# Kernel tuning notes

Hardware: AMD Instinct MI355X
Metric: run time of the kernel (lower is better)

The kernel has to match this reference:

```python
import jax, jax.numpy as jnp
import numpy as np

P = 32      # process_dim (event types)
H = 1024    # hidden_size
T = 128     # sequence length
B = 128     # batch size


def setup_inputs() -> dict:
    key = jax.random.key(0)
    k_dt, k_ty, k_e, k_w, k_b = jax.random.split(key, 5)
    seq_dt = jax.random.uniform(k_dt, (T, B), dtype=jnp.float32)
    seq_types = jax.random.randint(k_ty, (T, B), 0, P, dtype=jnp.int32)
    h0 = jnp.zeros((B, H), jnp.float32)
    c0 = jnp.zeros((B, H), jnp.float32)
    # Embedding: P+1 rows, padding row (index P) zeroed as in nn.Embedding(padding_idx=P)
    embed = (jax.random.normal(k_e, (P + 1, P), jnp.float32) * 0.02).at[P].set(0.0)
    # 7 gate Linears fused into one weight: order = [input, forget, output,
    # input_target, forget_target, z, decay]; torch Linear is y = v @ W^T + b,
    # here W is stored pre-transposed as [P+H, 7H].
    W = jax.random.normal(k_w, (P + H, 7 * H), jnp.float32) / np.sqrt(P + H)
    b = jax.random.normal(k_b, (7 * H,), jnp.float32) * 0.01
    return {"seq_dt": seq_dt, "seq_types": seq_types, "h0": h0, "c0": c0,
            "embed": embed, "W": W, "b": b}


def reference(seq_dt, seq_types, h0, c0, embed, W, b):
    def step(carry, inp):
        h_t, c_t, c_tgt = carry
        dt, types = inp                       # dt: [B], types: [B]
        x = embed[types]                      # [B, P]
        v = jnp.concatenate([x, h_t], axis=1) # [B, P+H]
        g = v @ W + b                         # fused 7-gate GEMM -> [B, 7H]
        gi, gf, go, git, gft, gz, gd = jnp.split(g, 7, axis=1)
        inpt = jax.nn.sigmoid(gi)
        forget = jax.nn.sigmoid(gf)
        output = jax.nn.sigmoid(go)
        in_tgt = jax.nn.sigmoid(git)
        fg_tgt = jax.nn.sigmoid(gft)
        z = jnp.tanh(gz)
        decay = jax.nn.softplus(8.0 * gd) / 8.0  # Softplus(beta=8)
        c_i = forget * c_t + inpt * z
        h_i = output * jnp.tanh(c_i)
        c_tgt_new = fg_tgt * c_tgt + in_tgt * z
        c_new = c_tgt_new + (c_i - c_tgt_new) * jnp.exp(-decay * dt[:, None])
        h_new = output * jnp.tanh(c_new)
        return (h_new, c_new, c_tgt_new), (h_i, h_new, output, c_i, c_tgt_new, decay)

    _, ys = jax.lax.scan(step, (h0, c0, c0), (seq_dt, seq_types))
    hiddens, hiddens_decayed, outputs, cells, cell_targets, decays = ys
    return hiddens, hiddens_decayed, outputs, cells, cell_targets, decays
```

## Files before the change

kernel.cpp:

```cpp
#include <hip/hip_runtime.h>
#include <hip/hip_bf16.h>

#define TT 128
#define BB 128
#define HH 1024
#define PP 32
#define G7 7168

typedef __attribute__((ext_vector_type(8))) short short8;
typedef __attribute__((ext_vector_type(4))) float f32x4;

__device__ __forceinline__ ushort f2bf(float f) {
    union { float f; unsigned int u; } v; v.f = f;
    unsigned int u = v.u;
    return (ushort)((u + 0x7FFFu + ((u >> 16) & 1u)) >> 16);
}
__device__ __forceinline__ float sigm(float x) { return 1.f / (1.f + __expf(-x)); }
__device__ __forceinline__ float ftanh(float x) {
    float e = __expf(2.f * x);
    return 1.f - 2.f / (e + 1.f);
}

__global__ void prep_w2(const float* __restrict__ W, ushort* __restrict__ W2) {
    int nt = blockIdx.x;
    int ki = blockIdx.y;
    int lane = threadIdx.x;
    int n = nt * 16 + (lane & 15);
    int k = ki * 32 + (lane >> 4) * 8;
    size_t off = ((size_t)(nt * 32 + ki) * 64 + lane) * 8;
    #pragma unroll
    for (int e = 0; e < 8; ++e)
        W2[off + e] = f2bf(W[(size_t)(32 + k + e) * G7 + n]);
}

__global__ void prep_g0(const float* __restrict__ W, const float* __restrict__ embed,
                        const float* __restrict__ bias, float* __restrict__ G0) {
    int n = blockIdx.x * 256 + threadIdx.x;
    int ty = blockIdx.y;
    float acc = bias[n];
    for (int p = 0; p < PP; ++p)
        acc += embed[ty * PP + p] * W[(size_t)p * G7 + n];
    G0[(size_t)ty * G7 + n] = acc;
}

__global__ void prep_init(const float* __restrict__ h0, const float* __restrict__ c0,
                          ushort* __restrict__ A4, float* __restrict__ c_state,
                          float* __restrict__ ctgt_state) {
    int i = blockIdx.x * 256 + threadIdx.x;
    int b = i >> 10, k = i & 1023;
    int lane = (b & 15) | (((k >> 3) & 3) << 4);
    size_t off = ((size_t)(((b >> 5) * 32 + (k >> 5)) * 2 + ((b >> 4) & 1)) * 64 + lane) * 8 + (k & 7);
    A4[off] = f2bf(h0[i]);
    c_state[i] = c0[i];
    ctgt_state[i] = c0[i];
}

__global__ __launch_bounds__(896) void step_kernel(
    const ushort* __restrict__ W2, const float* __restrict__ G0,
    const float* __restrict__ dts, const int* __restrict__ types,
    const ushort* __restrict__ a_read, ushort* __restrict__ a_write,
    float* __restrict__ c_state, float* __restrict__ ctgt_state,
    float* __restrict__ out, int t)
{
    __shared__ short8 Albuf[4096];
    __shared__ float gbuf[7][2][32][17];
    const int tid = threadIdx.x;
    const int wave = tid >> 6, lane = tid & 63;
    const int g = wave >> 1, kh = wave & 1;
    const int bid = blockIdx.x;
    const int ht = (bid & 7) * 8 + ((bid >> 3) & 7);
    const int bq = bid >> 6;

    const short8* Asrc = reinterpret_cast<const short8*>(a_read) + bq * 4096;
    #pragma unroll
    for (int r = 0; r < 4; ++r)
        Albuf[r * 896 + tid] = Asrc[r * 896 + tid];
    if (tid < 512) Albuf[3584 + tid] = Asrc[3584 + tid];
    __syncthreads();

    const short8* Wv = reinterpret_cast<const short8*>(W2)
                     + (size_t)(g * 64 + ht) * 2048 + (kh * 16) * 64 + lane;
    const short8* As = Albuf + (kh * 16) * 2 * 64 + lane;
    f32x4 acc0 = {}, acc1 = {};
    #pragma unroll 8
    for (int j = 0; j < 16; ++j) {
        short8 wf = Wv[j * 64];
        short8 a0 = As[(j * 2 + 0) * 64];
        short8 a1 = As[(j * 2 + 1) * 64];
        acc0 = __builtin_amdgcn_mfma_f32_16x16x32_bf16(a0, wf, acc0, 0, 0, 0);
        acc1 = __builtin_amdgcn_mfma_f32_16x16x32_bf16(a1, wf, acc1, 0, 0, 0);
    }

    {
        const int rb = (lane >> 4) * 4, lr = lane & 15;
        #pragma unroll
        for (int r = 0; r < 4; ++r) {
            gbuf[g][kh][rb + r][lr]      = acc0[r];
            gbuf[g][kh][16 + rb + r][lr] = acc1[r];
        }
    }
    __syncthreads();

    if (tid < 512) {
        const int br = tid >> 4, hc = tid & 15;
        const int b = bq * 32 + br;
        const int h = ht * 16 + hc;
        const int ty = types[t * BB + b];
        const float dt = dts[t * BB + b];
        const float* g0p = G0 + (size_t)ty * G7 + h;
        float pre[7];
        #pragma unroll
        for (int gg = 0; gg < 7; ++gg)
            pre[gg] = gbuf[gg][0][br][hc] + gbuf[gg][1][br][hc] + g0p[gg * HH];

        float inpt   = sigm(pre[0]);
        float forget = sigm(pre[1]);
        float output = sigm(pre[2]);
        float itg    = sigm(pre[3]);
        float ftg    = sigm(pre[4]);
        float z      = ftanh(pre[5]);
        float x8     = 8.f * pre[6];
        float sp     = fmaxf(x8, 0.f) + __logf(1.f + __expf(-fabsf(x8)));
        float decay  = sp * 0.125f;

        const size_t si = (size_t)b * HH + h;
        float c    = c_state[si];
        float ctgt = ctgt_state[si];
        float c_i      = forget * c + inpt * z;
        float h_i      = output * ftanh(c_i);
        float ctgt_new = ftg * ctgt + itg * z;
        float edt      = __expf(-decay * dt);
        float c_new    = ctgt_new + (c_i - ctgt_new) * edt;
        float h_new    = output * ftanh(c_new);

        const size_t OS = (size_t)TT * BB * HH;
        size_t ob = (size_t)t * BB * HH + si;
        __builtin_nontemporal_store(h_i,      &out[ob]);
        __builtin_nontemporal_store(h_new,    &out[OS + ob]);
        __builtin_nontemporal_store(output,   &out[2 * OS + ob]);
        __builtin_nontemporal_store(c_i,      &out[3 * OS + ob]);
        __builtin_nontemporal_store(ctgt_new, &out[4 * OS + ob]);
        __builtin_nontemporal_store(decay,    &out[5 * OS + ob]);
        c_state[si]    = c_new;
        ctgt_state[si] = ctgt_new;

        unsigned hb = (unsigned)f2bf(h_new);
        unsigned other = __shfl_down(hb, 1);
        if ((hc & 1) == 0) {
            int ki_w = h >> 5;
            int lane_w = (b & 15) | (((h >> 3) & 3) << 4);
            size_t aoff = ((size_t)((((b >> 5) * 32 + ki_w) * 2 + ((b >> 4) & 1)) * 64) + lane_w) * 8 + (h & 7);
            *reinterpret_cast<unsigned*>(a_write + aoff) = hb | (other << 16);
        }
    }
}

extern "C" void kernel_launch(void* const* d_in, const int* in_sizes, int n_in,
                              void* d_out, int out_size, void* d_ws, size_t ws_size,
                              hipStream_t stream) {
    const float* seq_dt    = (const float*)d_in[0];
    const int*   seq_types = (const int*)d_in[1];
    const float* h0        = (const float*)d_in[2];
    const float* c0        = (const float*)d_in[3];
    const float* embed     = (const float*)d_in[4];
    const float* W         = (const float*)d_in[5];
    const float* bias      = (const float*)d_in[6];
    float* out = (float*)d_out;

    char* ws = (char*)d_ws;
    ushort* W2  = (ushort*)ws;
    float*  G0b = (float*)(ws + 14680064);
    ushort* a40 = (ushort*)(ws + 15626240);
    ushort* a41 = (ushort*)(ws + 15888384);
    float*  cs  = (float*)(ws + 16150528);
    float*  cts = (float*)(ws + 16674816);

    hipLaunchKernelGGL(prep_w2, dim3(448, 32), dim3(64), 0, stream, W, W2);
    hipLaunchKernelGGL(prep_g0, dim3(28, 33), dim3(256), 0, stream, W, embed, bias, G0b);
    hipLaunchKernelGGL(prep_init, dim3(512), dim3(256), 0, stream, h0, c0, a40, cs, cts);

    for (int t = 0; t < TT; ++t) {
        const ushort* ar = (t & 1) ? a41 : a40;
        ushort*       aw = (t & 1) ? a40 : a41;
        hipLaunchKernelGGL(step_kernel, dim3(256), dim3(896), 0, stream,
                           W2, G0b, seq_dt, seq_types, ar, aw, cs, cts, out, t);
    }
}
```

Measured before the change: 829.4 us.

## Split batch tiles to 16 rows and double the step grid to 512 blocks

Each step block now covers 16 batch rows instead of 32, so the per-step grid grows from 256 to 512 blocks on a GPU with 256 CUs. The A-operand (hidden state) layout is changed to match, with one MFMA accumulator per wave instead of two. The aim is more parallelism and shorter per-block latency for the latency-bound recurrent step. The cost is that each bf16 weight tile is now read by twice as many blocks per step, which doubles weight traffic, and MFMA reuse of the loaded weight fragment drops.

```diff
diff --git a/kernel.cpp b/kernel.cpp
--- a/kernel.cpp
+++ b/kernel.cpp
@@ -44,66 +44,61 @@
 }
 
 __global__ void prep_init(const float* __restrict__ h0, const float* __restrict__ c0,
-                          ushort* __restrict__ A4, float* __restrict__ c_state,
+                          ushort* __restrict__ A5, float* __restrict__ c_state,
                           float* __restrict__ ctgt_state) {
     int i = blockIdx.x * 256 + threadIdx.x;
     int b = i >> 10, k = i & 1023;
     int lane = (b & 15) | (((k >> 3) & 3) << 4);
-    size_t off = ((size_t)(((b >> 5) * 32 + (k >> 5)) * 2 + ((b >> 4) & 1)) * 64 + lane) * 8 + (k & 7);
-    A4[off] = f2bf(h0[i]);
+    size_t off = (((size_t)(b >> 4) * 32 + (k >> 5)) * 64 + lane) * 8 + (k & 7);
+    A5[off] = f2bf(h0[i]);
     c_state[i] = c0[i];
     ctgt_state[i] = c0[i];
 }
 
-__global__ __launch_bounds__(896) void step_kernel(
+__global__ __launch_bounds__(896, 7) void step_kernel(
     const ushort* __restrict__ W2, const float* __restrict__ G0,
     const float* __restrict__ dts, const int* __restrict__ types,
     const ushort* __restrict__ a_read, ushort* __restrict__ a_write,
     float* __restrict__ c_state, float* __restrict__ ctgt_state,
     float* __restrict__ out, int t)
 {
-    __shared__ short8 Albuf[4096];
-    __shared__ float gbuf[7][2][32][17];
+    __shared__ short8 Albuf[2048];
+    __shared__ float gbuf[7][2][16][17];
     const int tid = threadIdx.x;
     const int wave = tid >> 6, lane = tid & 63;
     const int g = wave >> 1, kh = wave & 1;
     const int bid = blockIdx.x;
     const int ht = (bid & 7) * 8 + ((bid >> 3) & 7);
-    const int bq = bid >> 6;
+    const int bo = bid >> 6;
 
-    const short8* Asrc = reinterpret_cast<const short8*>(a_read) + bq * 4096;
-    #pragma unroll
-    for (int r = 0; r < 4; ++r)
-        Albuf[r * 896 + tid] = Asrc[r * 896 + tid];
-    if (tid < 512) Albuf[3584 + tid] = Asrc[3584 + tid];
+    const short8* Asrc = reinterpret_cast<const short8*>(a_read) + bo * 2048;
+    Albuf[tid] = Asrc[tid];
+    Albuf[896 + tid] = Asrc[896 + tid];
+    if (tid < 256) Albuf[1792 + tid] = Asrc[1792 + tid];
     __syncthreads();
 
     const short8* Wv = reinterpret_cast<const short8*>(W2)
                      + (size_t)(g * 64 + ht) * 2048 + (kh * 16) * 64 + lane;
-    const short8* As = Albuf + (kh * 16) * 2 * 64 + lane;
-    f32x4 acc0 = {}, acc1 = {};
+    const short8* As = Albuf + (kh * 16) * 64 + lane;
+    f32x4 acc = {};
     #pragma unroll 8
     for (int j = 0; j < 16; ++j) {
         short8 wf = Wv[j * 64];
-        short8 a0 = As[(j * 2 + 0) * 64];
-        short8 a1 = As[(j * 2 + 1) * 64];
-        acc0 = __builtin_amdgcn_mfma_f32_16x16x32_bf16(a0, wf, acc0, 0, 0, 0);
-        acc1 = __builtin_amdgcn_mfma_f32_16x16x32_bf16(a1, wf, acc1, 0, 0, 0);
+        short8 af = As[j * 64];
+        acc = __builtin_amdgcn_mfma_f32_16x16x32_bf16(af, wf, acc, 0, 0, 0);
     }
 
     {
         const int rb = (lane >> 4) * 4, lr = lane & 15;
         #pragma unroll
-        for (int r = 0; r < 4; ++r) {
-            gbuf[g][kh][rb + r][lr]      = acc0[r];
-            gbuf[g][kh][16 + rb + r][lr] = acc1[r];
-        }
+        for (int r = 0; r < 4; ++r)
+            gbuf[g][kh][rb + r][lr] = acc[r];
     }
     __syncthreads();
 
-    if (tid < 512) {
+    if (tid < 256) {
         const int br = tid >> 4, hc = tid & 15;
-        const int b = bq * 32 + br;
+        const int b = bo * 16 + br;
         const int h = ht * 16 + hc;
         const int ty = types[t * BB + b];
         const float dt = dts[t * BB + b];
@@ -149,7 +144,7 @@
         if ((hc & 1) == 0) {
             int ki_w = h >> 5;
             int lane_w = (b & 15) | (((h >> 3) & 3) << 4);
-            size_t aoff = ((size_t)((((b >> 5) * 32 + ki_w) * 2 + ((b >> 4) & 1)) * 64) + lane_w) * 8 + (h & 7);
+            size_t aoff = (((size_t)(b >> 4) * 32 + ki_w) * 64 + lane_w) * 8 + (h & 7);
             *reinterpret_cast<unsigned*>(a_write + aoff) = hb | (other << 16);
         }
     }
@@ -170,19 +165,19 @@
     char* ws = (char*)d_ws;
     ushort* W2  = (ushort*)ws;
     float*  G0b = (float*)(ws + 14680064);
-    ushort* a40 = (ushort*)(ws + 15626240);
-    ushort* a41 = (ushort*)(ws + 15888384);
+    ushort* a50 = (ushort*)(ws + 15626240);
+    ushort* a51 = (ushort*)(ws + 15888384);
     float*  cs  = (float*)(ws + 16150528);
     float*  cts = (float*)(ws + 16674816);
 
     hipLaunchKernelGGL(prep_w2, dim3(448, 32), dim3(64), 0, stream, W, W2);
     hipLaunchKernelGGL(prep_g0, dim3(28, 33), dim3(256), 0, stream, W, embed, bias, G0b);
-    hipLaunchKernelGGL(prep_init, dim3(512), dim3(256), 0, stream, h0, c0, a40, cs, cts);
+    hipLaunchKernelGGL(prep_init, dim3(512), dim3(256), 0, stream, h0, c0, a50, cs, cts);
 
     for (int t = 0; t < TT; ++t) {
-        const ushort* ar = (t & 1) ? a41 : a40;
-        ushort*       aw = (t & 1) ? a40 : a41;
-        hipLaunchKernelGGL(step_kernel, dim3(256), dim3(896), 0, stream,
+        const ushort* ar = (t & 1) ? a51 : a50;
+        ushort*       aw = (t & 1) ? a50 : a51;
+        hipLaunchKernelGGL(step_kernel, dim3(512), dim3(896), 0, stream,
                            W2, G0b, seq_dt, seq_types, ar, aw, cs, cts, out, t);
     }
 }
```

After: 1.080 ms. 1.3x slower.
